# Kernel optimization log

Hardware: AMD Instinct MI355X
Metric: run time of the kernel (lower is better)

Reference implementation:

```python
import jax, jax.numpy as jnp
import numpy as np

STRIDE = (1, 1)
PADDING = (1, 1)


def setup_inputs() -> dict:
    key = jax.random.key(0)
    k1, k2, k3 = jax.random.split(key, 3)
    x = jax.random.normal(k1, (32, 128, 56, 56), dtype=jnp.float32)
    # xavier_uniform for weight (out, in, kh, kw): bound = sqrt(6/(fan_in+fan_out))
    fan_in = 128 * 3 * 3
    fan_out = 256 * 3 * 3
    bound = float(np.sqrt(6.0 / (fan_in + fan_out)))
    weight = jax.random.uniform(k2, (256, 128, 3, 3), dtype=jnp.float32,
                                minval=-bound, maxval=bound)
    bias = jax.random.normal(k3, (256,), dtype=jnp.float32)
    return {"x": x, "weight": weight, "bias": bias}


def reference(x, weight, bias):
    # Faithful cross-correlation conv (torch semantics): NCHW input, OIHW weight.
    out = jax.lax.conv_general_dilated(
        x, weight,
        window_strides=STRIDE,
        padding=[(PADDING[0], PADDING[0]), (PADDING[1], PADDING[1])],
        dimension_numbers=("NCHW", "OIHW", "NCHW"),
    )
    out = out + bias[None, :, None, None]
    return out
```

## Files before the change

### kernel.cpp

```cpp
#include <hip/hip_runtime.h>
#include <cstdint>

typedef __bf16 bf16_t;
typedef __bf16 bf16x8 __attribute__((ext_vector_type(8)));
typedef float  f32x4  __attribute__((ext_vector_type(4)));

#define XPAD_ELEMS (32UL*58*58*128)
#define WPERM_OFF  (XPAD_ELEMS*2)
#define WPERM_ELEMS (256UL*9*128)
#define WS_NEEDED  (WPERM_OFF + WPERM_ELEMS*2)

__device__ __forceinline__ void async16(const bf16_t* g, const bf16_t* l) {
  __builtin_amdgcn_global_load_lds(
      (const __attribute__((address_space(1))) void*)g,
      (__attribute__((address_space(3))) void*)l, 16, 0, 0);
}

__global__ __launch_bounds__(256) void k_xform(const float* __restrict__ x, bf16_t* __restrict__ Xp) {
  const int b = blockIdx.x;
  const int n = b / 58, hp = b % 58;
  bf16_t* drow = Xp + ((size_t)n * 58 + hp) * 58 * 128;
  const int t = threadIdx.x;
  uint4 z; z.x = z.y = z.z = z.w = 0;
  if (hp == 0 || hp == 57) {
    uint4* p = (uint4*)drow;
    for (int i = t; i < 928; i += 256) p[i] = z;
    return;
  }
  if (t < 32) {
    uint4* p0 = (uint4*)drow;
    uint4* p1 = (uint4*)(drow + 57 * 128);
    if (t < 16) p0[t] = z; else p1[t - 16] = z;
  }
  const int h = hp - 1;
  const float* src = x + (size_t)n * 401408 + h * 56;
  __shared__ float lds[128 * 57];
  for (int i = t; i < 7168; i += 256) {
    int c = i / 56;
    int w = i - c * 56;
    lds[c * 57 + w] = src[(size_t)c * 3136 + w];
  }
  __syncthreads();
  bf16_t* dst = drow + 128;
  for (int i = t; i < 3584; i += 256) {
    int cp = i & 63, w = i >> 6;
    int c0 = cp * 2;
    unsigned short u0 = __builtin_bit_cast(unsigned short, (bf16_t)lds[c0 * 57 + w]);
    unsigned short u1 = __builtin_bit_cast(unsigned short, (bf16_t)lds[(c0 + 1) * 57 + w]);
    *(unsigned int*)(dst + (size_t)w * 128 + c0) = (unsigned)u0 | ((unsigned)u1 << 16);
  }
}

__global__ void k_wperm(const float* __restrict__ wt, bf16_t* __restrict__ Wp) {
  int i = blockIdx.x * 256 + threadIdx.x;
  if (i >= 294912) return;
  int e  = i & 7;
  int o  = (i >> 3) & 255;
  int kc = (i >> 11) & 3;
  int t  = i >> 13;
  int ci = t & 3, rs = t >> 2;
  int c  = ci * 32 + kc * 8 + e;
  Wp[i] = (bf16_t)wt[o * 1152 + c * 9 + rs];
}

__global__ void k_naive(const float* __restrict__ x, const float* __restrict__ wt,
                        const float* __restrict__ bs, float* __restrict__ out) {
  int idx = blockIdx.x * 256 + threadIdx.x;
  if (idx >= 25690112) return;
  int w = idx % 56; int tmp = idx / 56;
  int h = tmp % 56; tmp /= 56;
  int k = tmp % 256; int n = tmp / 256;
  float acc = bs[k];
  for (int c = 0; c < 128; ++c)
    for (int r = 0; r < 3; ++r) {
      int hy = h + r - 1; if ((unsigned)hy >= 56u) continue;
      for (int s = 0; s < 3; ++s) {
        int wx = w + s - 1; if ((unsigned)wx >= 56u) continue;
        acc += x[((size_t)(n * 128 + c) * 56 + hy) * 56 + wx] *
               wt[((size_t)(k * 128 + c) * 3 + r) * 3 + s];
      }
    }
  out[idx] = acc;
}

__global__ __launch_bounds__(256, 2) void k_conv(const bf16_t* __restrict__ Xp,
                                                 const bf16_t* __restrict__ Wpk,
                                                 const float* __restrict__ bias,
                                                 float* __restrict__ out) {
  __shared__ bf16_t strip[3712 * 8];
  const int tid = threadIdx.x, lane = tid & 63, wv = tid >> 6;
  const int sid = (int)blockIdx.x;
  const int n   = sid / 28;
  const int h0  = (sid - n * 28) * 2;

  const bf16_t* xrow = Xp + ((size_t)n * 58 + h0) * 58 * 128;
#pragma unroll
  for (int r = 0; r < 14; ++r) {
    int slot = r * 256 + tid;
    int pix = slot >> 4, cp = slot & 15;
    int hp = pix / 58, wp = pix - hp * 58;
    int cl = cp ^ (wp & 7);
    async16(xrow + ((size_t)(hp * 58 + wp)) * 128 + cl * 8,
            strip + (r * 256 + wv * 64) * 8);
  }
  if (tid < 128) {
    int slot = 3584 + tid;
    int pix = slot >> 4, cp = slot & 15;
    int hp = pix / 58, wp = pix - hp * 58;
    int cl = cp ^ (wp & 7);
    async16(xrow + ((size_t)(hp * 58 + wp)) * 128 + cl * 8,
            strip + (3584 + wv * 64) * 8);
  }

  const int fr = lane & 15, fg = lane >> 4;
  int pixb[7];
#pragma unroll
  for (int ni = 0; ni < 7; ++ni) {
    int pq = ni * 16 + fr;
    int oh = (pq >= 56) ? 1 : 0;
    pixb[ni] = pq + 2 * oh;
  }

  const bf16_t* wsrc = Wpk + fg * 2048 + (wv * 64 + fr) * 8;
  bf16x8 areg[2][4];
#pragma unroll
  for (int mi = 0; mi < 4; ++mi) {
    areg[0][mi] = *(const bf16x8*)(wsrc + mi * 128);
    areg[1][mi] = *(const bf16x8*)(wsrc + 8192 + mi * 128);
  }

  __syncthreads();

  f32x4 acc[4][7] = {};

#pragma unroll
  for (int t = 0; t < 36; ++t) {
    const int pb = t & 1;
    const int rs = t >> 2, ci = t & 3;
    const int r = rs / 3, s = rs - r * 3;
    const int cph = (ci * 4 + fg) ^ ((fr + s) & 7);
    const int base = ((r * 58 + s) * 16 + cph) * 8;

    bf16x8 bfr[7];
#pragma unroll
    for (int ni = 0; ni < 7; ++ni)
      bfr[ni] = *(const bf16x8*)&strip[pixb[ni] * 128 + base];
#pragma unroll
    for (int mi = 0; mi < 4; ++mi)
#pragma unroll
      for (int ni = 0; ni < 7; ++ni)
        acc[mi][ni] = __builtin_amdgcn_mfma_f32_16x16x32_bf16(areg[pb][mi], bfr[ni], acc[mi][ni], 0, 0, 0);
    if (t + 2 < 36) {
#pragma unroll
      for (int mi = 0; mi < 4; ++mi)
        areg[pb][mi] = *(const bf16x8*)(wsrc + (size_t)(t + 2) * 8192 + mi * 128);
    }
  }

  const int mbase = wv * 64;
  float bv[4][4];
#pragma unroll
  for (int mi = 0; mi < 4; ++mi)
#pragma unroll
    for (int j = 0; j < 4; ++j)
      bv[mi][j] = bias[mbase + mi * 16 + fg * 4 + j];

#pragma unroll
  for (int ni = 0; ni < 7; ++ni) {
    int pq = ni * 16 + fr;
    int oh = (pq >= 56) ? 1 : 0;
    int ow = pq - oh * 56;
    int h = h0 + oh;
    float* ob = out + (size_t)n * 802816 + h * 56 + ow;
#pragma unroll
    for (int mi = 0; mi < 4; ++mi) {
      int kb = mbase + mi * 16 + fg * 4;
#pragma unroll
      for (int j = 0; j < 4; ++j)
        ob[(size_t)(kb + j) * 3136] = acc[mi][ni][j] + bv[mi][j];
    }
  }
}

extern "C" void kernel_launch(void* const* d_in, const int* in_sizes, int n_in,
                              void* d_out, int out_size, void* d_ws, size_t ws_size,
                              hipStream_t stream) {
  const float* x  = (const float*)d_in[0];
  const float* wt = (const float*)d_in[1];
  const float* bs = (const float*)d_in[2];
  float* out = (float*)d_out;

  if (ws_size < WS_NEEDED) {
    k_naive<<<(25690112 + 255) / 256, 256, 0, stream>>>(x, wt, bs, out);
    return;
  }

  bf16_t* Xp  = (bf16_t*)d_ws;
  bf16_t* Wpk = (bf16_t*)((char*)d_ws + WPERM_OFF);

  k_xform<<<1856, 256, 0, stream>>>(x, Xp);
  k_wperm<<<1152, 256, 0, stream>>>(wt, Wpk);
  k_conv <<<896, 256, 0, stream>>>(Xp, Wpk, bs, out);
}
```

Baseline: 79.19 us.

## Tile conv output as 8x8 spatial patches with 10x10 halo strip

New measurement: 121.8 us. +53.8%, slower.

```diff
diff --git a/kernel.cpp b/kernel.cpp
--- a/kernel.cpp
+++ b/kernel.cpp
@@ -83,45 +83,48 @@
   out[idx] = acc;
 }
 
-__global__ __launch_bounds__(256, 2) void k_conv(const bf16_t* __restrict__ Xp,
+__global__ __launch_bounds__(256, 4) void k_conv(const bf16_t* __restrict__ Xp,
                                                  const bf16_t* __restrict__ Wpk,
                                                  const float* __restrict__ bias,
                                                  float* __restrict__ out) {
-  __shared__ bf16_t strip[3712 * 8];
+  __shared__ bf16_t strip[1600 * 8];
   const int tid = threadIdx.x, lane = tid & 63, wv = tid >> 6;
-  const int sid = (int)blockIdx.x;
-  const int n   = sid / 28;
-  const int h0  = (sid - n * 28) * 2;
-
-  const bf16_t* xrow = Xp + ((size_t)n * 58 + h0) * 58 * 128;
-#pragma unroll
-  for (int r = 0; r < 14; ++r) {
-    int slot = r * 256 + tid;
-    int pix = slot >> 4, cp = slot & 15;
-    int hp = pix / 58, wp = pix - hp * 58;
-    int cl = cp ^ (wp & 7);
-    async16(xrow + ((size_t)(hp * 58 + wp)) * 128 + cl * 8,
-            strip + (r * 256 + wv * 64) * 8);
-  }
-  if (tid < 128) {
-    int slot = 3584 + tid;
-    int pix = slot >> 4, cp = slot & 15;
-    int hp = pix / 58, wp = pix - hp * 58;
-    int cl = cp ^ (wp & 7);
-    async16(xrow + ((size_t)(hp * 58 + wp)) * 128 + cl * 8,
-            strip + (3584 + wv * 64) * 8);
+  const int bid = (int)blockIdx.x;
+  const int n   = bid / 49;
+  const int rem = bid - n * 49;
+  const int ph0 = (rem / 7) * 8;
+  const int pw0 = (rem % 7) * 8;
+
+  const bf16_t* xpatch = Xp + (((size_t)n * 58 + ph0) * 58 + pw0) * 128;
+#pragma unroll
+  for (int rr = 0; rr < 6; ++rr) {
+    int slot = rr * 256 + tid;
+    int lp = slot >> 4, cp = slot & 15;
+    int ph = lp / 10, pw = lp - ph * 10;
+    int cl = cp ^ ((ph * 8 + pw) & 15);
+    async16(xpatch + ((size_t)ph * 58 + pw) * 128 + cl * 8,
+            strip + (rr * 256 + wv * 64) * 8);
+  }
+  if (wv == 0) {
+    int slot = 1536 + lane;
+    int lp = slot >> 4, cp = slot & 15;
+    int ph = lp / 10, pw = lp - ph * 10;
+    int cl = cp ^ ((ph * 8 + pw) & 15);
+    async16(xpatch + ((size_t)ph * 58 + pw) * 128 + cl * 8,
+            strip + 1536 * 8);
   }
 
   const int fr = lane & 15, fg = lane >> 4;
-  int pixb[7];
-#pragma unroll
-  for (int ni = 0; ni < 7; ++ni) {
-    int pq = ni * 16 + fr;
-    int oh = (pq >= 56) ? 1 : 0;
-    pixb[ni] = pq + 2 * oh;
-  }
-
-  const bf16_t* wsrc = Wpk + fg * 2048 + (wv * 64 + fr) * 8;
+  const int prl = fr >> 3, pcl = fr & 7;
+  int poff[4], fb[4];
+#pragma unroll
+  for (int ni = 0; ni < 4; ++ni) {
+    int prow = 2 * ni + prl;
+    poff[ni] = (prow * 10 + pcl) * 128;
+    fb[ni]   = prow * 8 + pcl;
+  }
+
+  const bf16_t* wsrc = Wpk + fg * 2048 + ((wv << 6) + fr) * 8;
   bf16x8 areg[2][4];
 #pragma unroll
   for (int mi = 0; mi < 4; ++mi) {
@@ -131,25 +134,30 @@
 
   __syncthreads();
 
-  f32x4 acc[4][7] = {};
+  f32x4 acc[4][4] = {};
 
 #pragma unroll
   for (int t = 0; t < 36; ++t) {
     const int pb = t & 1;
     const int rs = t >> 2, ci = t & 3;
     const int r = rs / 3, s = rs - r * 3;
-    const int cph = (ci * 4 + fg) ^ ((fr + s) & 7);
-    const int base = ((r * 58 + s) * 16 + cph) * 8;
-
-    bf16x8 bfr[7];
-#pragma unroll
-    for (int ni = 0; ni < 7; ++ni)
-      bfr[ni] = *(const bf16x8*)&strip[pixb[ni] * 128 + base];
+    const int pixAdd = (r * 10 + s) * 128;
+    const int fAdd = r * 8 + s;
+    const int clbase = ci * 4;
+
+    bf16x8 bfr[4];
+#pragma unroll
+    for (int ni = 0; ni < 4; ++ni) {
+      int cp = (clbase ^ fg) ^ ((fb[ni] + fAdd) & 15);
+      bfr[ni] = *(const bf16x8*)&strip[poff[ni] + pixAdd + cp * 8];
+    }
+    __builtin_amdgcn_s_setprio(1);
 #pragma unroll
     for (int mi = 0; mi < 4; ++mi)
 #pragma unroll
-      for (int ni = 0; ni < 7; ++ni)
+      for (int ni = 0; ni < 4; ++ni)
         acc[mi][ni] = __builtin_amdgcn_mfma_f32_16x16x32_bf16(areg[pb][mi], bfr[ni], acc[mi][ni], 0, 0, 0);
+    __builtin_amdgcn_s_setprio(0);
     if (t + 2 < 36) {
 #pragma unroll
       for (int mi = 0; mi < 4; ++mi)
@@ -166,12 +174,9 @@
       bv[mi][j] = bias[mbase + mi * 16 + fg * 4 + j];
 
 #pragma unroll
-  for (int ni = 0; ni < 7; ++ni) {
-    int pq = ni * 16 + fr;
-    int oh = (pq >= 56) ? 1 : 0;
-    int ow = pq - oh * 56;
-    int h = h0 + oh;
-    float* ob = out + (size_t)n * 802816 + h * 56 + ow;
+  for (int ni = 0; ni < 4; ++ni) {
+    int pr = 2 * ni + prl;
+    float* ob = out + (size_t)n * 802816 + (ph0 + pr) * 56 + (pw0 + pcl);
 #pragma unroll
     for (int mi = 0; mi < 4; ++mi) {
       int kb = mbase + mi * 16 + fg * 4;
@@ -200,5 +205,5 @@
 
   k_xform<<<1856, 256, 0, stream>>>(x, Xp);
   k_wperm<<<1152, 256, 0, stream>>>(wt, Wpk);
-  k_conv <<<896, 256, 0, stream>>>(Xp, Wpk, bs, out);
-}
+  k_conv <<<1568, 256, 0, stream>>>(Xp, Wpk, bs, out);
+}
```

## Enlarge conv block to 4 rows with LDS-staged triple-buffered weights

Applied to the files above, without the earlier changes.

New measurement: 101.9 us. +28.7%, slower.

```diff
diff --git a/kernel.cpp b/kernel.cpp
--- a/kernel.cpp
+++ b/kernel.cpp
@@ -83,81 +83,98 @@
   out[idx] = acc;
 }
 
-__global__ __launch_bounds__(256, 2) void k_conv(const bf16_t* __restrict__ Xp,
+__global__ __launch_bounds__(512, 2) void k_conv(const bf16_t* __restrict__ Xp,
                                                  const bf16_t* __restrict__ Wpk,
                                                  const float* __restrict__ bias,
                                                  float* __restrict__ out) {
-  __shared__ bf16_t strip[3712 * 8];
+  __shared__ bf16_t strip[5568 * 8];
+  __shared__ bf16_t Alds[3][8192];
   const int tid = threadIdx.x, lane = tid & 63, wv = tid >> 6;
   const int sid = (int)blockIdx.x;
-  const int n   = sid / 28;
-  const int h0  = (sid - n * 28) * 2;
+  const int n   = sid / 14;
+  const int h0  = (sid - n * 14) * 4;
 
   const bf16_t* xrow = Xp + ((size_t)n * 58 + h0) * 58 * 128;
 #pragma unroll
-  for (int r = 0; r < 14; ++r) {
-    int slot = r * 256 + tid;
+  for (int r = 0; r < 10; ++r) {
+    int slot = r * 512 + tid;
     int pix = slot >> 4, cp = slot & 15;
     int hp = pix / 58, wp = pix - hp * 58;
     int cl = cp ^ (wp & 7);
     async16(xrow + ((size_t)(hp * 58 + wp)) * 128 + cl * 8,
-            strip + (r * 256 + wv * 64) * 8);
-  }
-  if (tid < 128) {
-    int slot = 3584 + tid;
+            strip + (r * 512 + wv * 64) * 8);
+  }
+  if (tid < 448) {
+    int slot = 5120 + tid;
     int pix = slot >> 4, cp = slot & 15;
     int hp = pix / 58, wp = pix - hp * 58;
     int cl = cp ^ (wp & 7);
     async16(xrow + ((size_t)(hp * 58 + wp)) * 128 + cl * 8,
-            strip + (3584 + wv * 64) * 8);
-  }
+            strip + (5120 + wv * 64) * 8);
+  }
+
+#define STAGE_A(buf, tt) do {                                              \
+    async16(Wpk + (size_t)(tt) * 8192 + (0 * 512 + tid) * 8,               \
+            &Alds[buf][(0 * 512 + wv * 64) * 8]);                          \
+    async16(Wpk + (size_t)(tt) * 8192 + (1 * 512 + tid) * 8,               \
+            &Alds[buf][(1 * 512 + wv * 64) * 8]);                          \
+  } while (0)
+
+  STAGE_A(0, 0);
+  STAGE_A(1, 1);
 
   const int fr = lane & 15, fg = lane >> 4;
-  int pixb[7];
+  const int pg = wv & 1, cg = wv >> 1;
+  int pixoff[7];
 #pragma unroll
   for (int ni = 0; ni < 7; ++ni) {
-    int pq = ni * 16 + fr;
-    int oh = (pq >= 56) ? 1 : 0;
-    pixb[ni] = pq + 2 * oh;
-  }
-
-  const bf16_t* wsrc = Wpk + fg * 2048 + (wv * 64 + fr) * 8;
-  bf16x8 areg[2][4];
-#pragma unroll
-  for (int mi = 0; mi < 4; ++mi) {
-    areg[0][mi] = *(const bf16x8*)(wsrc + mi * 128);
-    areg[1][mi] = *(const bf16x8*)(wsrc + 8192 + mi * 128);
-  }
-
-  __syncthreads();
+    int pq = pg * 112 + ni * 16 + fr;
+    int oh = pq / 56;
+    pixoff[ni] = (pq + 2 * oh) * 128;
+  }
+  const int abase = (fg * 256 + cg * 64 + fr) * 8;
+
+  asm volatile("s_waitcnt vmcnt(2)" ::: "memory");
+  __builtin_amdgcn_s_barrier();
+  __builtin_amdgcn_sched_barrier(0);
 
   f32x4 acc[4][7] = {};
 
 #pragma unroll
   for (int t = 0; t < 36; ++t) {
-    const int pb = t & 1;
+    const int cur = t % 3;
+    if (t + 2 < 36) STAGE_A((t + 2) % 3, t + 2);
     const int rs = t >> 2, ci = t & 3;
     const int r = rs / 3, s = rs - r * 3;
-    const int cph = (ci * 4 + fg) ^ ((fr + s) & 7);
-    const int base = ((r * 58 + s) * 16 + cph) * 8;
-
-    bf16x8 bfr[7];
-#pragma unroll
-    for (int ni = 0; ni < 7; ++ni)
-      bfr[ni] = *(const bf16x8*)&strip[pixb[ni] * 128 + base];
+    const int pixAdd = (r * 58 + s) * 128;
+    const int cphv = ci * 4;
+
+    bf16x8 afr[4], bfr[7];
 #pragma unroll
     for (int mi = 0; mi < 4; ++mi)
+      afr[mi] = *(const bf16x8*)&Alds[cur][abase + mi * 128];
+#pragma unroll
+    for (int ni = 0; ni < 7; ++ni) {
+      int cph = (cphv + fg) ^ ((fr + s) & 7);
+      bfr[ni] = *(const bf16x8*)&strip[pixoff[ni] + pixAdd + cph * 8];
+    }
+    __builtin_amdgcn_s_setprio(1);
+#pragma unroll
+    for (int mi = 0; mi < 4; ++mi)
 #pragma unroll
       for (int ni = 0; ni < 7; ++ni)
-        acc[mi][ni] = __builtin_amdgcn_mfma_f32_16x16x32_bf16(areg[pb][mi], bfr[ni], acc[mi][ni], 0, 0, 0);
-    if (t + 2 < 36) {
-#pragma unroll
-      for (int mi = 0; mi < 4; ++mi)
-        areg[pb][mi] = *(const bf16x8*)(wsrc + (size_t)(t + 2) * 8192 + mi * 128);
-    }
-  }
-
-  const int mbase = wv * 64;
+        acc[mi][ni] = __builtin_amdgcn_mfma_f32_16x16x32_bf16(afr[mi], bfr[ni], acc[mi][ni], 0, 0, 0);
+    __builtin_amdgcn_s_setprio(0);
+    if (t < 35) {
+      if (t < 34) asm volatile("s_waitcnt vmcnt(2)" ::: "memory");
+      else        asm volatile("s_waitcnt vmcnt(0)" ::: "memory");
+      __builtin_amdgcn_s_barrier();
+      __builtin_amdgcn_sched_barrier(0);
+    }
+  }
+#undef STAGE_A
+
+  const int mbase = cg * 64;
   float bv[4][4];
 #pragma unroll
   for (int mi = 0; mi < 4; ++mi)
@@ -167,11 +184,10 @@
 
 #pragma unroll
   for (int ni = 0; ni < 7; ++ni) {
-    int pq = ni * 16 + fr;
-    int oh = (pq >= 56) ? 1 : 0;
+    int pq = pg * 112 + ni * 16 + fr;
+    int oh = pq / 56;
     int ow = pq - oh * 56;
-    int h = h0 + oh;
-    float* ob = out + (size_t)n * 802816 + h * 56 + ow;
+    float* ob = out + (size_t)n * 802816 + (h0 + oh) * 56 + ow;
 #pragma unroll
     for (int mi = 0; mi < 4; ++mi) {
       int kb = mbase + mi * 16 + fg * 4;
@@ -200,5 +216,5 @@
 
   k_xform<<<1856, 256, 0, stream>>>(x, Xp);
   k_wperm<<<1152, 256, 0, stream>>>(wt, Wpk);
-  k_conv <<<896, 256, 0, stream>>>(Xp, Wpk, bs, out);
-}
+  k_conv <<<448, 512, 0, stream>>>(Xp, Wpk, bs, out);
+}
```
